# Kernel optimization log

Hardware: AMD Instinct MI355X
Metric: run time of the kernel (lower is better)

Reference implementation:

```python
import jax, jax.numpy as jnp
import numpy as np

N, K, CONV_DIM = 100, 20, 256
TEMP, ALPHA = 0.1, 0.1
B_NORM = 1  # module hardcodes self.B = 1
BATCH = 8


def setup_inputs() -> dict:
    key = jax.random.key(0)
    inputs = jax.random.normal(key, (BATCH, N, K, CONV_DIM), dtype=jnp.float32)
    return {"inputs": inputs}


def reference(inputs) -> jnp.ndarray:
    # inputs: [B, N, K, D] prototype representations
    B, n, k, D = inputs.shape
    # L2-normalize along feature dim (reduce_euclidean_norm)
    xn = inputs / jnp.sqrt(jnp.sum(inputs * inputs, axis=-1, keepdims=True))
    flat = xn.reshape(B, n * k, D)  # all prototypes, all classes: [B, N*K, D]

    # anchor-vs-all similarities: [B, N, K, N*K]
    sims = jnp.einsum('bnkd,bmd->bnkm', xn, flat) / TEMP
    # anchor self-similarity (==1/t after normalization, but keep exact math): [B, N, K]
    self_sim = jnp.sum(xn * xn, axis=-1) / TEMP

    # denominator: sum_m exp(sim) - exp(self)
    denom = jnp.sum(jnp.exp(sims), axis=-1) - jnp.exp(self_sim)
    log_term = jnp.log(denom)  # [B, N, K]

    # intra-class similarity sum: anchor vs all K prototypes of its own class
    intra = jnp.einsum('bnkd,bnjd->bnk', xn, xn) / TEMP  # [B, N, K]
    sum_term = (intra - self_sim) / (k - 1)

    cl_loss = jnp.sum(log_term - sum_term)  # summed over batch and all N*K anchors
    loss = ALPHA * cl_loss / (B_NORM * n * k * D)
    return loss
```

## Files before the change

### kernel.cpp

```cpp
#include <hip/hip_runtime.h>
#include <math.h>

#define BB 8
#define NN 100
#define KK 20
#define DD 256
#define MM 2000
#define MP 2048
#define NTILE 136
#define GRID2 (BB * NTILE)
#define NSLICE 32
#define TINV 10.0f
#define LOSS_SCALE 1.953125e-7f

typedef __bf16 bf16x8 __attribute__((ext_vector_type(8)));
typedef float floatx4 __attribute__((ext_vector_type(4)));
typedef __attribute__((address_space(1))) const ushort GUshort;
typedef __attribute__((address_space(3))) ushort LUshort;

__device__ __forceinline__ ushort f2bf(float f) {
    unsigned int u = __float_as_uint(f);
    u += 0x7fffu + ((u >> 16) & 1u);
    return (ushort)(u >> 16);
}

__device__ __forceinline__ void agent_store(float* p, float v) {
    __hip_atomic_store(p, v, __ATOMIC_RELAXED, __HIP_MEMORY_SCOPE_AGENT);
}
__device__ __forceinline__ float agent_load(const float* p) {
    return __hip_atomic_load(p, __ATOMIC_RELAXED, __HIP_MEMORY_SCOPE_AGENT);
}

__global__ void norm_bf16(const float* __restrict__ x, ushort* __restrict__ xb,
                          unsigned int* __restrict__ ctr, float* __restrict__ out) {
    if (blockIdx.x == 0 && threadIdx.x < BB) ctr[threadIdx.x * 16] = 0u;
    if (blockIdx.x == 0 && threadIdx.x == 0) out[0] = 0.0f;

    const int rg = blockIdx.x * 4 + (threadIdx.x >> 6);
    const int lane = threadIdx.x & 63;
    const int b = rg >> 11;
    const int r = rg & (MP - 1);
    ushort4 outv = make_ushort4(0, 0, 0, 0);
    if (r < MM) {
        const float4 v = ((const float4*)(x + ((size_t)(b * MM + r)) * DD))[lane];
        float s = v.x * v.x + v.y * v.y + v.z * v.z + v.w * v.w;
        #pragma unroll
        for (int o = 32; o >= 1; o >>= 1) s += __shfl_xor(s, o, 64);
        const float inv = 1.0f / sqrtf(s);
        outv.x = f2bf(v.x * inv);
        outv.y = f2bf(v.y * inv);
        outv.z = f2bf(v.z * inv);
        outv.w = f2bf(v.w * inv);
    }
    ((ushort4*)(xb + (size_t)rg * DD))[lane] = outv;
}

__global__ __launch_bounds__(256)
void cl_mfma(const ushort* __restrict__ xb,
             float* __restrict__ deS, float* __restrict__ itS,
             unsigned int* __restrict__ ctr, float* __restrict__ out) {
    __shared__ __align__(16) ushort As[128 * 64];
    __shared__ __align__(16) ushort Bs[128 * 64];

    const int b = blockIdx.x & 7;
    int rem = blockIdx.x >> 3;
    int ti = 0;
    while (rem >= 16 - ti) { rem -= 16 - ti; ++ti; }
    const int tj = ti + rem;
    const int rbase = ti << 7;
    const int cbase = tj << 7;
    const bool offdiag = (ti != tj);
    const ushort* __restrict__ xbb = xb + (size_t)b * MP * DD;

    const int tid = threadIdx.x;
    const int lane = tid & 63;
    const int w = tid >> 6;
    const int wr = (w >> 1) << 6;
    const int wc = (w & 1) << 6;
    const int tx = lane & 15;
    const int tx7 = tx & 7;
    const int quad = lane >> 4;

    const int srow = lane >> 3;
    const int sg = (lane & 7) ^ srow;

    floatx4 acc[4][4];
    #pragma unroll
    for (int mt = 0; mt < 4; ++mt)
        #pragma unroll
        for (int nt = 0; nt < 4; ++nt)
            acc[mt][nt] = (floatx4){0.f, 0.f, 0.f, 0.f};

    #pragma unroll 1
    for (int kc = 0; kc < 4; ++kc) {
        __syncthreads();
        #pragma unroll
        for (int q = 0; q < 4; ++q) {
            const int R = ((w << 2) + q) << 3;
            const size_t koff = (kc << 6) + (sg << 3);
            __builtin_amdgcn_global_load_lds(
                (GUshort*)(xbb + (size_t)(rbase + R + srow) * DD + koff),
                (LUshort*)(As + R * 64), 16, 0, 0);
            __builtin_amdgcn_global_load_lds(
                (GUshort*)(xbb + (size_t)(cbase + R + srow) * DD + koff),
                (LUshort*)(Bs + R * 64), 16, 0, 0);
        }
        __syncthreads();

        #pragma unroll
        for (int ks = 0; ks < 2; ++ks) {
            const int g = (ks << 2) + quad;
            const int gp = (g ^ tx7) << 3;
            bf16x8 af[4], bf[4];
            #pragma unroll
            for (int mt = 0; mt < 4; ++mt)
                af[mt] = *(const bf16x8*)(As + (wr + (mt << 4) + tx) * 64 + gp);
            #pragma unroll
            for (int nt = 0; nt < 4; ++nt)
                bf[nt] = *(const bf16x8*)(Bs + (wc + (nt << 4) + tx) * 64 + gp);
            #pragma unroll
            for (int mt = 0; mt < 4; ++mt)
                #pragma unroll
                for (int nt = 0; nt < 4; ++nt)
                    acc[mt][nt] = __builtin_amdgcn_mfma_f32_16x16x32_bf16(af[mt], bf[nt], acc[mt][nt], 0, 0, 0);
        }
    }

    int colv[4], colcls[4];
    bool colok[4];
    #pragma unroll
    for (int nt = 0; nt < 4; ++nt) {
        const int c = cbase + wc + (nt << 4) + tx;
        colv[nt] = c;
        colok[nt] = c < MM;
        colcls[nt] = c / KK;
    }
    float de_c[4] = {0.f, 0.f, 0.f, 0.f};
    float it_c[4] = {0.f, 0.f, 0.f, 0.f};

    float* __restrict__ deR = deS + ((size_t)(((tj << 1) | (w & 1)) * BB + b)) * MP;
    float* __restrict__ itR = itS + ((size_t)(((tj << 1) | (w & 1)) * BB + b)) * MP;
    float* __restrict__ deC = deS + ((size_t)(((ti << 1) | (w >> 1)) * BB + b)) * MP;
    float* __restrict__ itC = itS + ((size_t)(((ti << 1) | (w >> 1)) * BB + b)) * MP;

    #pragma unroll
    for (int mt = 0; mt < 4; ++mt) {
        #pragma unroll
        for (int i = 0; i < 4; ++i) {
            const int row = rbase + wr + (mt << 4) + (quad << 2) + i;
            const int rcls = row / KK;
            float de = 0.f, it = 0.f;
            #pragma unroll
            for (int nt = 0; nt < 4; ++nt) {
                const float sim = acc[mt][nt][i] * TINV;
                const bool ok = colok[nt] && (colv[nt] != row);
                const float e = ok ? __expf(sim) : 0.0f;
                const float sv = (ok && (colcls[nt] == rcls)) ? sim : 0.0f;
                de += e;
                it += sv;
                de_c[nt] += e;
                it_c[nt] += sv;
            }
            #pragma unroll
            for (int o = 8; o >= 1; o >>= 1) {
                de += __shfl_xor(de, o, 64);
                it += __shfl_xor(it, o, 64);
            }
            if (tx == 0) {
                agent_store(&deR[row], de);
                agent_store(&itR[row], it);
            }
        }
    }

    if (offdiag) {
        #pragma unroll
        for (int nt = 0; nt < 4; ++nt) {
            de_c[nt] += __shfl_xor(de_c[nt], 16, 64);
            de_c[nt] += __shfl_xor(de_c[nt], 32, 64);
            it_c[nt] += __shfl_xor(it_c[nt], 16, 64);
            it_c[nt] += __shfl_xor(it_c[nt], 32, 64);
        }
        if (quad == 0) {
            #pragma unroll
            for (int nt = 0; nt < 4; ++nt) {
                agent_store(&deC[colv[nt]], de_c[nt]);
                agent_store(&itC[colv[nt]], it_c[nt]);
            }
        }
    }

    __syncthreads();
    unsigned int* tick = (unsigned int*)As;
    if (tid == 0) tick[0] = atomicAdd(&ctr[b * 16], 1u);
    __syncthreads();
    if (tick[0] == NTILE - 1) {
        float s = 0.0f;
        #pragma unroll 1
        for (int k = 0; k < 8; ++k) {
            const int r2 = tid + (k << 8);
            float dsum = 0.0f, isum = 0.0f;
            #pragma unroll
            for (int sl = 0; sl < NSLICE; ++sl) {
                dsum += agent_load(deS + ((size_t)(sl * BB + b)) * MP + r2);
                isum += agent_load(itS + ((size_t)(sl * BB + b)) * MP + r2);
            }
            const float t = logf(dsum) - isum * (1.0f / (KK - 1));
            s += (r2 < MM) ? t : 0.0f;
        }
        #pragma unroll
        for (int o = 32; o >= 1; o >>= 1) s += __shfl_xor(s, o, 64);
        float* red = (float*)(As + 128);
        if (lane == 0) red[w] = s;
        __syncthreads();
        if (tid == 0)
            atomicAdd(out, (red[0] + red[1] + red[2] + red[3]) * LOSS_SCALE);
    }
}

extern "C" void kernel_launch(void* const* d_in, const int* in_sizes, int n_in,
                              void* d_out, int out_size, void* d_ws, size_t ws_size,
                              hipStream_t stream) {
    const float* x = (const float*)d_in[0];
    float* out = (float*)d_out;
    float* deS = (float*)d_ws;
    float* itS = deS + NSLICE * BB * MP;
    ushort* xb = (ushort*)(itS + NSLICE * BB * MP);
    unsigned int* ctr = (unsigned int*)(xb + (size_t)BB * MP * DD);

    norm_bf16<<<BB * MP / 4, 256, 0, stream>>>(x, xb, ctr, out);
    cl_mfma<<<GRID2, 256, 0, stream>>>(xb, deS, itS, ctr, out);
}
```

Measured before the change: 103.5 us.

## Double-buffer LDS K-slices to overlap global loads with MFMA compute

After: 100.5 us. -2.9%, faster.

```diff
diff --git a/kernel.cpp b/kernel.cpp
--- a/kernel.cpp
+++ b/kernel.cpp
@@ -59,8 +59,8 @@
 void cl_mfma(const ushort* __restrict__ xb,
              float* __restrict__ deS, float* __restrict__ itS,
              unsigned int* __restrict__ ctr, float* __restrict__ out) {
-    __shared__ __align__(16) ushort As[128 * 64];
-    __shared__ __align__(16) ushort Bs[128 * 64];
+    __shared__ __align__(16) ushort As[2][128 * 32];
+    __shared__ __align__(16) ushort Bs[2][128 * 32];
 
     const int b = blockIdx.x & 7;
     int rem = blockIdx.x >> 3;
@@ -78,11 +78,13 @@
     const int wr = (w >> 1) << 6;
     const int wc = (w & 1) << 6;
     const int tx = lane & 15;
-    const int tx7 = tx & 7;
     const int quad = lane >> 4;
 
-    const int srow = lane >> 3;
-    const int sg = (lane & 7) ^ srow;
+    const int srow4 = lane >> 2;
+    const int slot4 = lane & 3;
+    const int sg4 = slot4 ^ ((lane >> 3) & 3);
+
+    const int slot8 = (quad ^ ((tx >> 1) & 3)) << 3;
 
     floatx4 acc[4][4];
     #pragma unroll
@@ -91,40 +93,51 @@
         for (int nt = 0; nt < 4; ++nt)
             acc[mt][nt] = (floatx4){0.f, 0.f, 0.f, 0.f};
 
-    #pragma unroll 1
-    for (int kc = 0; kc < 4; ++kc) {
-        __syncthreads();
-        #pragma unroll
-        for (int q = 0; q < 4; ++q) {
-            const int R = ((w << 2) + q) << 3;
-            const size_t koff = (kc << 6) + (sg << 3);
-            __builtin_amdgcn_global_load_lds(
-                (GUshort*)(xbb + (size_t)(rbase + R + srow) * DD + koff),
-                (LUshort*)(As + R * 64), 16, 0, 0);
-            __builtin_amdgcn_global_load_lds(
-                (GUshort*)(xbb + (size_t)(cbase + R + srow) * DD + koff),
-                (LUshort*)(Bs + R * 64), 16, 0, 0);
-        }
-        __syncthreads();
-
-        #pragma unroll
-        for (int ks = 0; ks < 2; ++ks) {
-            const int g = (ks << 2) + quad;
-            const int gp = (g ^ tx7) << 3;
-            bf16x8 af[4], bf[4];
-            #pragma unroll
-            for (int mt = 0; mt < 4; ++mt)
-                af[mt] = *(const bf16x8*)(As + (wr + (mt << 4) + tx) * 64 + gp);
-            #pragma unroll
-            for (int nt = 0; nt < 4; ++nt)
-                bf[nt] = *(const bf16x8*)(Bs + (wc + (nt << 4) + tx) * 64 + gp);
-            #pragma unroll
-            for (int mt = 0; mt < 4; ++mt)
-                #pragma unroll
-                for (int nt = 0; nt < 4; ++nt)
-                    acc[mt][nt] = __builtin_amdgcn_mfma_f32_16x16x32_bf16(af[mt], bf[nt], acc[mt][nt], 0, 0, 0);
-        }
-    }
+#define STAGE(P, T)                                                                  \
+    {                                                                                \
+        _Pragma("unroll")                                                            \
+        for (int h = 0; h < 2; ++h) {                                                \
+            const int R = (w << 5) + (h << 4);                                       \
+            const size_t koff = ((size_t)(T) << 5) + (sg4 << 3);                     \
+            __builtin_amdgcn_global_load_lds(                                        \
+                (GUshort*)(xbb + (size_t)(rbase + R + srow4) * DD + koff),           \
+                (LUshort*)(&As[P][R * 32]), 16, 0, 0);                               \
+            __builtin_amdgcn_global_load_lds(                                        \
+                (GUshort*)(xbb + (size_t)(cbase + R + srow4) * DD + koff),           \
+                (LUshort*)(&Bs[P][R * 32]), 16, 0, 0);                               \
+        }                                                                            \
+    }
+
+#define COMPUTE(P)                                                                   \
+    {                                                                                \
+        bf16x8 af[4], bf[4];                                                         \
+        _Pragma("unroll")                                                            \
+        for (int mt = 0; mt < 4; ++mt)                                               \
+            af[mt] = *(const bf16x8*)(&As[P][(wr + (mt << 4) + tx) * 32 + slot8]);   \
+        _Pragma("unroll")                                                            \
+        for (int nt = 0; nt < 4; ++nt)                                               \
+            bf[nt] = *(const bf16x8*)(&Bs[P][(wc + (nt << 4) + tx) * 32 + slot8]);   \
+        _Pragma("unroll")                                                            \
+        for (int mt = 0; mt < 4; ++mt)                                               \
+            _Pragma("unroll")                                                        \
+            for (int nt = 0; nt < 4; ++nt)                                           \
+                acc[mt][nt] = __builtin_amdgcn_mfma_f32_16x16x32_bf16(               \
+                    af[mt], bf[nt], acc[mt][nt], 0, 0, 0);                           \
+    }
+
+    STAGE(0, 0);
+    __syncthreads();
+    STAGE(1, 1); COMPUTE(0); __syncthreads();
+    STAGE(0, 2); COMPUTE(1); __syncthreads();
+    STAGE(1, 3); COMPUTE(0); __syncthreads();
+    STAGE(0, 4); COMPUTE(1); __syncthreads();
+    STAGE(1, 5); COMPUTE(0); __syncthreads();
+    STAGE(0, 6); COMPUTE(1); __syncthreads();
+    STAGE(1, 7); COMPUTE(0); __syncthreads();
+    COMPUTE(1);
+
+#undef STAGE
+#undef COMPUTE
 
     int colv[4], colcls[4];
     bool colok[4];
@@ -191,7 +204,7 @@
     }
 
     __syncthreads();
-    unsigned int* tick = (unsigned int*)As;
+    unsigned int* tick = (unsigned int*)&As[0][0];
     if (tid == 0) tick[0] = atomicAdd(&ctr[b * 16], 1u);
     __syncthreads();
     if (tick[0] == NTILE - 1) {
@@ -210,7 +223,7 @@
         }
         #pragma unroll
         for (int o = 32; o >= 1; o >>= 1) s += __shfl_xor(s, o, 64);
-        float* red = (float*)(As + 128);
+        float* red = (float*)(&As[0][128]);
         if (lane == 0) red[w] = s;
         __syncthreads();
         if (tid == 0)
```
